# Kernel tuning notes

Hardware: AMD Instinct MI355X
Metric: run time of the kernel (lower is better)

The kernel has to match this reference:

```python
import jax, jax.numpy as jnp
import numpy as np

# Static config (must match init_kwargs)
IMG_H, IMG_W = 48, 160
BEV_H, BEV_W = 128, 128
X_MIN, X_MAX, Y_MIN, Y_MAX = -51.2, 51.2, -51.2, 51.2
RES_X = (X_MAX - X_MIN) / BEV_W
RES_Y = (Y_MAX - Y_MIN) / BEV_H
C, D, B = 128, 64, 2


def setup_inputs() -> dict:
    key = jax.random.key(0)
    k1, k2, k3, k4 = jax.random.split(key, 4)
    img_features = jax.random.normal(k1, (B, C, IMG_H, IMG_W), dtype=jnp.float32)
    # depth distribution per pixel (softmax over D, as a depth net would emit)
    depth_probs = jax.nn.softmax(jax.random.normal(k2, (B, D, IMG_H, IMG_W), dtype=jnp.float32), axis=1)
    # depth bin centers: 1m .. 60m
    depth_values = jnp.linspace(1.0, 60.0, D, dtype=jnp.float32)
    # realistic pinhole intrinsics (feature-map scale) with tiny per-cam jitter
    fx, fy, cx, cy = 120.0, 120.0, IMG_W / 2.0, IMG_H / 2.0
    K0 = jnp.array([[fx, 0.0, cx], [0.0, fy, cy], [0.0, 0.0, 1.0]], dtype=jnp.float32)
    K = K0[None] + 0.01 * jax.random.normal(k3, (B, 3, 3), dtype=jnp.float32) * jnp.array(
        [[1.0, 0.0, 1.0], [0.0, 1.0, 1.0], [0.0, 0.0, 0.0]], dtype=jnp.float32)
    # cam->lidar extrinsic: cam z (forward) -> lidar x, cam x -> -lidar y, cam y -> -lidar z
    R0 = jnp.array([[0.0, 0.0, 1.0], [-1.0, 0.0, 0.0], [0.0, -1.0, 0.0]], dtype=jnp.float32)
    t0 = jnp.array([1.5, 0.0, 1.8], dtype=jnp.float32)
    T0 = jnp.eye(4, dtype=jnp.float32).at[:3, :3].set(R0).at[:3, 3].set(t0)
    T = T0[None] + jnp.zeros((B, 4, 4), dtype=jnp.float32)
    T = T.at[:, :3, 3].add(0.05 * jax.random.normal(k4, (B, 3), dtype=jnp.float32))
    return {"img_features": img_features, "depth_probs": depth_probs,
            "depth_values": depth_values, "K": K, "T": T}


def _lss_forward(img_features, depth_probs, depth_values, K, T):
    Bn, Cn, H, W = img_features.shape
    Dn = depth_values.shape[0]
    # homogeneous pixel grid [H, W, 3]
    gx, gy = jnp.meshgrid(jnp.arange(W, dtype=jnp.float32),
                          jnp.arange(H, dtype=jnp.float32), indexing="xy")
    grid = jnp.stack([gx, gy, jnp.ones_like(gx)], axis=-1)
    # unproject: rays [B, H, W, 3]
    K_inv = jnp.linalg.inv(K)
    rays = jnp.einsum("bij,hwj->bhwi", K_inv, grid)
    # points in camera frame [B, D, H, W, 3]
    pts_cam = depth_values[None, :, None, None, None] * rays[:, None]
    # camera -> lidar
    pts = jnp.einsum("bij,bdhwj->bdhwi", T[:, :3, :3], pts_cam) + T[:, None, None, None, :3, 3]
    x, y, z = pts[..., 0], pts[..., 1], pts[..., 2]
    # torch .long() truncates toward zero -> astype int32 matches
    bx = ((x - X_MIN) / RES_X).astype(jnp.int32)
    by = ((y - Y_MIN) / RES_Y).astype(jnp.int32)
    valid = (bx >= 0) & (bx < BEV_W) & (by >= 0) & (by < BEV_H) & (z > 0)
    # depth-weighted features [B, D, H, W, C], masked instead of gathered
    weighted = jnp.einsum("bchw,bdhw->bdhwc", img_features, depth_probs)
    weighted = weighted * valid[..., None]
    idx = jnp.where(valid, by * BEV_W + bx, 0).reshape(Bn, -1)
    feats = weighted.reshape(Bn, -1, Cn)
    bev_flat = jax.vmap(lambda f, i: jax.ops.segment_sum(f, i, num_segments=BEV_H * BEV_W))(feats, idx)
    return bev_flat.reshape(Bn, BEV_H, BEV_W, Cn).transpose(0, 3, 1, 2)


def reference(img_features, depth_probs, depth_values, K, T):
    return _lss_forward(img_features, depth_probs, depth_values, K, T)
```

## Files before the change

kernel.cpp:

```cpp
#include <hip/hip_runtime.h>

constexpr int IMG_H = 48, IMG_W = 160;
constexpr int HW    = IMG_H * IMG_W;
constexpr int BEV_H = 128, BEV_W = 128;
constexpr int NCELL = BEV_H * BEV_W;
constexpr int C_DIM = 128, D_DIM = 64, B_DIM = 2;
constexpr int NCELL_TOT = B_DIM * NCELL;
constexpr int NPIX_TOT  = B_DIM * HW;
constexpr int NPTS      = NPIX_TOT * D_DIM;
constexpr int MAX_ENTRIES = NPTS;
constexpr int CHUNK = 64;
constexpr int NSHARD = 16;
constexpr float X_MIN = -51.2f, Y_MIN = -51.2f;
constexpr float RES_X = 102.4f / 128.0f;
constexpr float RES_Y = 102.4f / 128.0f;

constexpr size_t WS_IMG_T = 0;
constexpr size_t WS_HIST2 = WS_IMG_T + (size_t)B_DIM * HW * C_DIM;
constexpr size_t WS_OUT_T = WS_HIST2 + (size_t)NSHARD * NCELL_TOT;
constexpr size_t WS_HIST  = WS_OUT_T + (size_t)NCELL_TOT * C_DIM;
constexpr size_t WS_OFFS  = WS_HIST + NCELL_TOT;
constexpr size_t WS_EKEY  = WS_OFFS + NCELL_TOT + 4;
constexpr size_t WS_EW16  = WS_EKEY + MAX_ENTRIES;
constexpr size_t WS_NEED_CM = (WS_EW16 + MAX_ENTRIES / 2) * 4;

__device__ inline int point_shard(int tid) {
    return ((tid >> 2) + (tid >> 8)) & (NSHARD - 1);
}

__device__ inline void make_ray(const float* __restrict__ K, int b, float gx, float gy,
                                float& rx, float& ry, float& rz) {
    const float* Kb = K + b * 9;
    const float a00 = Kb[0], a01 = Kb[1], a02 = Kb[2];
    const float a10 = Kb[3], a11 = Kb[4], a12 = Kb[5];
    const float a20 = Kb[6], a21 = Kb[7], a22 = Kb[8];
    const float det = a00 * (a11 * a22 - a12 * a21)
                    - a01 * (a10 * a22 - a12 * a20)
                    + a02 * (a10 * a21 - a11 * a20);
    const float inv = 1.0f / det;
    const float i00 =  (a11 * a22 - a12 * a21) * inv;
    const float i01 = -(a01 * a22 - a02 * a21) * inv;
    const float i02 =  (a01 * a12 - a02 * a11) * inv;
    const float i10 = -(a10 * a22 - a12 * a20) * inv;
    const float i11 =  (a00 * a22 - a02 * a20) * inv;
    const float i12 = -(a00 * a12 - a02 * a10) * inv;
    const float i20 =  (a10 * a21 - a11 * a20) * inv;
    const float i21 = -(a00 * a21 - a01 * a20) * inv;
    const float i22 =  (a00 * a11 - a01 * a10) * inv;
    rx = i00 * gx + i01 * gy + i02;
    ry = i10 * gx + i11 * gy + i12;
    rz = i20 * gx + i21 * gy + i22;
}

__device__ inline int point_gcell(int tid, const float* __restrict__ dv,
                                  const float* __restrict__ K,
                                  const float* __restrict__ T) {
    const int pix = tid % HW;
    const int bd  = tid / HW;
    const int d   = bd % D_DIM;
    const int b   = bd / D_DIM;
    const int h = pix / IMG_W, w = pix % IMG_W;
    float rx, ry, rz;
    make_ray(K, b, (float)w, (float)h, rx, ry, rz);
    const float* Tb = T + b * 16;
    const float dep = dv[d];
    const float px = dep * rx, py = dep * ry, pz = dep * rz;
    const float x = Tb[0] * px + Tb[1] * py + Tb[2]  * pz + Tb[3];
    const float y = Tb[4] * px + Tb[5] * py + Tb[6]  * pz + Tb[7];
    const float z = Tb[8] * px + Tb[9] * py + Tb[10] * pz + Tb[11];
    const int bx = (int)((x - X_MIN) / RES_X);
    const int by = (int)((y - Y_MIN) / RES_Y);
    const bool valid = (bx >= 0) && (bx < BEV_W) && (by >= 0) && (by < BEV_H) && (z > 0.0f);
    return valid ? (b * NCELL + by * BEV_W + bx) : -1;
}

__device__ inline bool wave_runs(int gcell, int lane, int& run_len, int& leader_idx) {
    const int left = __shfl_up(gcell, 1);
    const bool is_leader = (lane == 0) || (left != gcell);
    const unsigned long long lmask = __ballot(is_leader);
    const unsigned long long rest = (lane == 63) ? 0ULL : (lmask >> (lane + 1));
    const int f = __ffsll((unsigned long long)rest);
    run_len = f ? f : (64 - lane);
    const unsigned long long below =
        lmask & ((lane == 63) ? ~0ULL : ((1ULL << (lane + 1)) - 1ULL));
    leader_idx = 63 - __clzll((long long)below);
    return is_leader;
}

__global__ __launch_bounds__(256) void k_transpose(const float* __restrict__ img,
                                                   float* __restrict__ img_t) {
    __shared__ float tile[32][33];
    const int b = blockIdx.z;
    const int tx = threadIdx.x, ty = threadIdx.y;
    const int pix0 = blockIdx.x * 32, c0 = blockIdx.y * 32;
    #pragma unroll
    for (int j = 0; j < 32; j += 8)
        tile[ty + j][tx] = img[((size_t)(b * C_DIM + c0 + ty + j)) * HW + pix0 + tx];
    __syncthreads();
    #pragma unroll
    for (int j = 0; j < 32; j += 8)
        img_t[((size_t)(b * HW + pix0 + ty + j)) * C_DIM + c0 + tx] = tile[tx][ty + j];
}

__global__ __launch_bounds__(256) void k_count(const float* __restrict__ dv,
                                               const float* __restrict__ K,
                                               const float* __restrict__ T,
                                               int* __restrict__ hist2) {
    const int tid = blockIdx.x * 256 + threadIdx.x;
    const int gcell = point_gcell(tid, dv, K, T);
    const int lane = threadIdx.x & 63;
    int run_len, leader_idx;
    const bool lead = wave_runs(gcell, lane, run_len, leader_idx);
    if (lead && gcell >= 0)
        atomicAdd(&hist2[(size_t)point_shard(tid) * NCELL_TOT + gcell], run_len);
}

__global__ __launch_bounds__(256) void k_reduce(const int* __restrict__ hist2,
                                                int* __restrict__ hist) {
    const int cell = blockIdx.x * 256 + threadIdx.x;
    int s = 0;
    #pragma unroll
    for (int sh = 0; sh < NSHARD; ++sh)
        s += hist2[(size_t)sh * NCELL_TOT + cell];
    hist[cell] = s;
}

__global__ __launch_bounds__(1024) void k_scan(const int* __restrict__ hist,
                                               int* __restrict__ offs) {
    __shared__ int lds[1024];
    const int t = threadIdx.x;
    int h[32];
    int s = 0;
    const int base = t * 32;
    #pragma unroll
    for (int k = 0; k < 32; ++k) { h[k] = hist[base + k]; s += h[k]; }
    lds[t] = s;
    __syncthreads();
    for (int off = 1; off < 1024; off <<= 1) {
        int v = (t >= off) ? lds[t - off] : 0;
        __syncthreads();
        lds[t] += v;
        __syncthreads();
    }
    int run = lds[t] - s;
    #pragma unroll
    for (int k = 0; k < 32; ++k) {
        offs[base + k] = run;
        run += h[k];
    }
    if (t == 1023) offs[NCELL_TOT] = lds[1023];
}

__global__ __launch_bounds__(256) void k_shardbase(int* __restrict__ hist2,
                                                   const int* __restrict__ offs) {
    const int cell = blockIdx.x * 256 + threadIdx.x;
    int run = offs[cell];
    #pragma unroll
    for (int sh = 0; sh < NSHARD; ++sh) {
        const size_t idx = (size_t)sh * NCELL_TOT + cell;
        const int cnt = hist2[idx];
        hist2[idx] = run;
        run += cnt;
    }
}

__global__ __launch_bounds__(256) void k_fill(const float* __restrict__ dp,
                                              const float* __restrict__ dv,
                                              const float* __restrict__ K,
                                              const float* __restrict__ T,
                                              int* __restrict__ cursor2,
                                              int* __restrict__ ekey,
                                              unsigned short* __restrict__ ew16) {
    const int tid = blockIdx.x * 256 + threadIdx.x;
    const int gcell = point_gcell(tid, dv, K, T);
    const int lane = threadIdx.x & 63;
    int run_len, leader_idx;
    const bool lead = wave_runs(gcell, lane, run_len, leader_idx);
    int base = 0;
    if (lead && gcell >= 0)
        base = atomicAdd(&cursor2[(size_t)point_shard(tid) * NCELL_TOT + gcell], run_len);
    base = __shfl(base, leader_idx);
    if (gcell < 0) return;
    const int slot = base + (lane - leader_idx);
    const float p = dp[tid];
    ekey[slot] = (gcell << 13) | (tid % HW);
    ew16[slot] = (unsigned short)__float2uint_rn(p * 65535.0f);
}

template <bool CELL_MAJOR>
__global__ __launch_bounds__(64) void k_chunk_gather(
    const float* __restrict__ img_t,
    const int* __restrict__ offs,
    const int* __restrict__ ekey,
    const unsigned short* __restrict__ ew16,
    float* __restrict__ acc_out)
{
    const int total = offs[NCELL_TOT];
    const int base = blockIdx.x * CHUNK;
    if (base >= total) return;

    __shared__ int   s_key[CHUNK];
    __shared__ float s_w[CHUNK];
    {
        const int i = threadIdx.x;
        const int idx = min(base + i, total - 1);
        s_key[i] = ekey[idx];
        s_w[i]   = (base + i < total) ? (float)ew16[base + i] * (1.0f / 65535.0f)
                                      : 0.0f;
    }
    __syncthreads();

    const int c2 = threadIdx.x * 2;
    int prev = s_key[0] >> 13;
    float2 acc = make_float2(0.0f, 0.0f);
    #pragma unroll 8
    for (int k = 0; k < CHUNK; ++k) {
        const int key = s_key[k];
        const float wgt = s_w[k];
        const int gcell = key >> 13;
        const int pix = key & 8191;
        const int b = gcell >> 14;
        const float2 v = *reinterpret_cast<const float2*>(
            &img_t[((size_t)(b * HW + pix)) * C_DIM + c2]);
        if (gcell != prev) {
            if (CELL_MAJOR) {
                float* o = &acc_out[(size_t)prev * C_DIM + c2];
                atomicAdd(o, acc.x);
                atomicAdd(o + 1, acc.y);
            } else {
                const int pb = prev >> 14, pc = prev & (NCELL - 1);
                float* o = &acc_out[((size_t)(pb * C_DIM + c2)) * NCELL + pc];
                atomicAdd(o, acc.x);
                atomicAdd(o + NCELL, acc.y);
            }
            acc = make_float2(0.0f, 0.0f);
            prev = gcell;
        }
        acc.x = fmaf(v.x, wgt, acc.x);
        acc.y = fmaf(v.y, wgt, acc.y);
    }
    if (CELL_MAJOR) {
        float* o = &acc_out[(size_t)prev * C_DIM + c2];
        atomicAdd(o, acc.x);
        atomicAdd(o + 1, acc.y);
    } else {
        const int pb = prev >> 14, pc = prev & (NCELL - 1);
        float* o = &acc_out[((size_t)(pb * C_DIM + c2)) * NCELL + pc];
        atomicAdd(o, acc.x);
        atomicAdd(o + NCELL, acc.y);
    }
}

__global__ __launch_bounds__(256) void k_untranspose(const float* __restrict__ out_t,
                                                     float* __restrict__ out) {
    __shared__ float tile[32][33];
    const int b = blockIdx.z;
    const int tx = threadIdx.x, ty = threadIdx.y;
    const int cell0 = blockIdx.x * 32, c0 = blockIdx.y * 32;
    const float* src = out_t + (size_t)b * NCELL * C_DIM;
    #pragma unroll
    for (int j = 0; j < 32; j += 8)
        tile[ty + j][tx] = src[((size_t)(cell0 + ty + j)) * C_DIM + c0 + tx];
    __syncthreads();
    #pragma unroll
    for (int j = 0; j < 32; j += 8)
        out[((size_t)(b * C_DIM + c0 + ty + j)) * NCELL + cell0 + tx] = tile[tx][ty + j];
}

extern "C" void kernel_launch(void* const* d_in, const int* in_sizes, int n_in,
                              void* d_out, int out_size, void* d_ws, size_t ws_size,
                              hipStream_t stream) {
    const float* img = (const float*)d_in[0];
    const float* dp  = (const float*)d_in[1];
    const float* dv  = (const float*)d_in[2];
    const float* K   = (const float*)d_in[3];
    const float* T   = (const float*)d_in[4];
    float* out = (float*)d_out;

    float* ws_f   = (float*)d_ws;
    float* img_t  = ws_f + WS_IMG_T;
    int*   hist2  = (int*)d_ws + WS_HIST2;
    float* out_t  = ws_f + WS_OUT_T;
    int*   hist   = (int*)d_ws + WS_HIST;
    int*   offs   = (int*)d_ws + WS_OFFS;
    int*   ekey   = (int*)d_ws + WS_EKEY;
    unsigned short* ew16 = (unsigned short*)((int*)d_ws + WS_EW16);

    const bool cell_major = (ws_size >= WS_NEED_CM);

    if (cell_major) {
        hipMemsetAsync(hist2, 0,
                       ((size_t)NSHARD * NCELL_TOT + (size_t)NCELL_TOT * C_DIM) * sizeof(int),
                       stream);
    } else {
        hipMemsetAsync(hist2, 0, (size_t)NSHARD * NCELL_TOT * sizeof(int), stream);
        hipMemsetAsync(out, 0, (size_t)out_size * sizeof(float), stream);
    }

    k_transpose<<<dim3(HW / 32, C_DIM / 32, B_DIM), dim3(32, 8), 0, stream>>>(img, img_t);
    k_count<<<NPTS / 256, 256, 0, stream>>>(dv, K, T, hist2);
    k_reduce<<<NCELL_TOT / 256, 256, 0, stream>>>(hist2, hist);
    k_scan<<<1, 1024, 0, stream>>>(hist, offs);
    k_shardbase<<<NCELL_TOT / 256, 256, 0, stream>>>(hist2, offs);
    k_fill<<<NPTS / 256, 256, 0, stream>>>(dp, dv, K, T, hist2, ekey, ew16);
    if (cell_major) {
        k_chunk_gather<true><<<MAX_ENTRIES / CHUNK, 64, 0, stream>>>(
            img_t, offs, ekey, ew16, out_t);
        k_untranspose<<<dim3(NCELL / 32, C_DIM / 32, B_DIM), dim3(32, 8), 0, stream>>>(
            out_t, out);
    } else {
        k_chunk_gather<false><<<MAX_ENTRIES / CHUNK, 64, 0, stream>>>(
            img_t, offs, ekey, ew16, out);
    }
}
```

Measured before the change: 164.7 us.

## Pre-merge depth bins per pixel ray and fuse transposes with counting

```diff
diff --git a/kernel.cpp b/kernel.cpp
--- a/kernel.cpp
+++ b/kernel.cpp
@@ -8,25 +8,22 @@
 constexpr int NCELL_TOT = B_DIM * NCELL;
 constexpr int NPIX_TOT  = B_DIM * HW;
 constexpr int NPTS      = NPIX_TOT * D_DIM;
-constexpr int MAX_ENTRIES = NPTS;
 constexpr int CHUNK = 64;
-constexpr int NSHARD = 16;
+constexpr int NSHARD = 64;
+constexpr int GATHER_BLOCKS = 3840;
+constexpr int CHUNKS_PER_BLOCK = NPTS / CHUNK / GATHER_BLOCKS;
 constexpr float X_MIN = -51.2f, Y_MIN = -51.2f;
 constexpr float RES_X = 102.4f / 128.0f;
 constexpr float RES_Y = 102.4f / 128.0f;
 
 constexpr size_t WS_IMG_T = 0;
-constexpr size_t WS_HIST2 = WS_IMG_T + (size_t)B_DIM * HW * C_DIM;
+constexpr size_t WS_DP_T  = WS_IMG_T + (size_t)B_DIM * HW * C_DIM;
+constexpr size_t WS_HIST2 = WS_DP_T + (size_t)B_DIM * HW * D_DIM;
 constexpr size_t WS_OUT_T = WS_HIST2 + (size_t)NSHARD * NCELL_TOT;
 constexpr size_t WS_HIST  = WS_OUT_T + (size_t)NCELL_TOT * C_DIM;
 constexpr size_t WS_OFFS  = WS_HIST + NCELL_TOT;
 constexpr size_t WS_EKEY  = WS_OFFS + NCELL_TOT + 4;
-constexpr size_t WS_EW16  = WS_EKEY + MAX_ENTRIES;
-constexpr size_t WS_NEED_CM = (WS_EW16 + MAX_ENTRIES / 2) * 4;
-
-__device__ inline int point_shard(int tid) {
-    return ((tid >> 2) + (tid >> 8)) & (NSHARD - 1);
-}
+constexpr size_t WS_EW16  = WS_EKEY + NPTS;
 
 __device__ inline void make_ray(const float* __restrict__ K, int b, float gx, float gy,
                                 float& rx, float& ry, float& rz) {
@@ -52,13 +49,10 @@
     rz = i20 * gx + i21 * gy + i22;
 }
 
-__device__ inline int point_gcell(int tid, const float* __restrict__ dv,
-                                  const float* __restrict__ K,
-                                  const float* __restrict__ T) {
-    const int pix = tid % HW;
-    const int bd  = tid / HW;
-    const int d   = bd % D_DIM;
-    const int b   = bd / D_DIM;
+__device__ inline int gcell_ray(int b, int pix, int d,
+                                const float* __restrict__ dv,
+                                const float* __restrict__ K,
+                                const float* __restrict__ T) {
     const int h = pix / IMG_W, w = pix % IMG_W;
     float rx, ry, rz;
     make_ray(K, b, (float)w, (float)h, rx, ry, rz);
@@ -74,45 +68,61 @@
     return valid ? (b * NCELL + by * BEV_W + bx) : -1;
 }
 
-__device__ inline bool wave_runs(int gcell, int lane, int& run_len, int& leader_idx) {
+struct RunInfo { int leader_idx; bool is_tail; };
+__device__ inline RunInfo wave_runs_d(int gcell, int lane) {
     const int left = __shfl_up(gcell, 1);
     const bool is_leader = (lane == 0) || (left != gcell);
     const unsigned long long lmask = __ballot(is_leader);
-    const unsigned long long rest = (lane == 63) ? 0ULL : (lmask >> (lane + 1));
-    const int f = __ffsll((unsigned long long)rest);
-    run_len = f ? f : (64 - lane);
     const unsigned long long below =
         lmask & ((lane == 63) ? ~0ULL : ((1ULL << (lane + 1)) - 1ULL));
-    leader_idx = 63 - __clzll((long long)below);
-    return is_leader;
-}
-
-__global__ __launch_bounds__(256) void k_transpose(const float* __restrict__ img,
-                                                   float* __restrict__ img_t) {
-    __shared__ float tile[32][33];
-    const int b = blockIdx.z;
-    const int tx = threadIdx.x, ty = threadIdx.y;
-    const int pix0 = blockIdx.x * 32, c0 = blockIdx.y * 32;
-    #pragma unroll
-    for (int j = 0; j < 32; j += 8)
-        tile[ty + j][tx] = img[((size_t)(b * C_DIM + c0 + ty + j)) * HW + pix0 + tx];
-    __syncthreads();
-    #pragma unroll
-    for (int j = 0; j < 32; j += 8)
-        img_t[((size_t)(b * HW + pix0 + ty + j)) * C_DIM + c0 + tx] = tile[tx][ty + j];
-}
-
-__global__ __launch_bounds__(256) void k_count(const float* __restrict__ dv,
-                                               const float* __restrict__ K,
-                                               const float* __restrict__ T,
-                                               int* __restrict__ hist2) {
-    const int tid = blockIdx.x * 256 + threadIdx.x;
-    const int gcell = point_gcell(tid, dv, K, T);
-    const int lane = threadIdx.x & 63;
-    int run_len, leader_idx;
-    const bool lead = wave_runs(gcell, lane, run_len, leader_idx);
-    if (lead && gcell >= 0)
-        atomicAdd(&hist2[(size_t)point_shard(tid) * NCELL_TOT + gcell], run_len);
+    RunInfo r;
+    r.leader_idx = 63 - __clzll((long long)below);
+    r.is_tail = (lane == 63) || ((lmask >> (lane + 1)) & 1ULL);
+    return r;
+}
+
+__device__ inline int shard_of(int pix) { return (pix ^ (pix >> 6)) & (NSHARD - 1); }
+
+constexpr int NB_IMG = (HW / 32) * (C_DIM / 32) * B_DIM;
+constexpr int NB_DP  = (HW / 32) * (D_DIM / 32) * B_DIM;
+constexpr int NB_CNT = NPTS / 256;
+__global__ __launch_bounds__(256) void k_prep(const float* __restrict__ img,
+                                              const float* __restrict__ dp,
+                                              const float* __restrict__ dv,
+                                              const float* __restrict__ K,
+                                              const float* __restrict__ T,
+                                              float* __restrict__ img_t,
+                                              float* __restrict__ dp_t,
+                                              int* __restrict__ hist2) {
+    int bid = blockIdx.x;
+    if (bid < NB_IMG + NB_DP) {
+        const float* src; float* dst; int rows;
+        if (bid < NB_IMG) { src = img; dst = img_t; rows = C_DIM; }
+        else              { bid -= NB_IMG; src = dp; dst = dp_t; rows = D_DIM; }
+        const int tiles_c = rows / 32;
+        const int b = bid / ((HW / 32) * tiles_c);
+        const int r = bid % ((HW / 32) * tiles_c);
+        const int ctile = r / (HW / 32), ptile = r % (HW / 32);
+        __shared__ float tile[32][33];
+        const int tx = threadIdx.x & 31, ty = threadIdx.x >> 5;
+        const int pix0 = ptile * 32, c0 = ctile * 32;
+        #pragma unroll
+        for (int j = 0; j < 32; j += 8)
+            tile[ty + j][tx] = src[((size_t)(b * rows + c0 + ty + j)) * HW + pix0 + tx];
+        __syncthreads();
+        #pragma unroll
+        for (int j = 0; j < 32; j += 8)
+            dst[((size_t)(b * HW + pix0 + ty + j)) * rows + c0 + tx] = tile[tx][ty + j];
+    } else {
+        const int tid = (bid - NB_IMG - NB_DP) * 256 + threadIdx.x;
+        const int lane = threadIdx.x & 63;
+        const int wid = tid >> 6;
+        const int b = wid / HW, pix = wid % HW;
+        const int gcell = gcell_ray(b, pix, lane, dv, K, T);
+        const RunInfo ri = wave_runs_d(gcell, lane);
+        if (ri.is_tail && gcell >= 0)
+            atomicAdd(&hist2[(size_t)shard_of(pix) * NCELL_TOT + gcell], 1);
+    }
 }
 
 __global__ __launch_bounds__(256) void k_reduce(const int* __restrict__ hist2,
@@ -164,7 +174,7 @@
     }
 }
 
-__global__ __launch_bounds__(256) void k_fill(const float* __restrict__ dp,
+__global__ __launch_bounds__(256) void k_fill(const float* __restrict__ dp_t,
                                               const float* __restrict__ dv,
                                               const float* __restrict__ K,
                                               const float* __restrict__ T,
@@ -172,82 +182,77 @@
                                               int* __restrict__ ekey,
                                               unsigned short* __restrict__ ew16) {
     const int tid = blockIdx.x * 256 + threadIdx.x;
-    const int gcell = point_gcell(tid, dv, K, T);
     const int lane = threadIdx.x & 63;
-    int run_len, leader_idx;
-    const bool lead = wave_runs(gcell, lane, run_len, leader_idx);
-    int base = 0;
-    if (lead && gcell >= 0)
-        base = atomicAdd(&cursor2[(size_t)point_shard(tid) * NCELL_TOT + gcell], run_len);
-    base = __shfl(base, leader_idx);
-    if (gcell < 0) return;
-    const int slot = base + (lane - leader_idx);
-    const float p = dp[tid];
-    ekey[slot] = (gcell << 13) | (tid % HW);
-    ew16[slot] = (unsigned short)__float2uint_rn(p * 65535.0f);
-}
-
-template <bool CELL_MAJOR>
-__global__ __launch_bounds__(64) void k_chunk_gather(
+    const int wid = tid >> 6;
+    const int b = wid / HW, pix = wid % HW;
+    const int gcell = gcell_ray(b, pix, lane, dv, K, T);
+    const RunInfo ri = wave_runs_d(gcell, lane);
+    const float p = dp_t[((size_t)(b * HW + pix)) * D_DIM + lane];
+    float val = p;
+    #pragma unroll
+    for (int dlt = 1; dlt < 64; dlt <<= 1) {
+        const float up = __shfl_up(val, dlt);
+        val = (lane - dlt >= ri.leader_idx) ? val + up : val;
+    }
+    if (ri.is_tail && gcell >= 0) {
+        const int slot = atomicAdd(&cursor2[(size_t)shard_of(pix) * NCELL_TOT + gcell], 1);
+        ekey[slot] = (gcell << 13) | pix;
+        ew16[slot] = (unsigned short)__float2uint_rn(fminf(val * 65535.0f, 65535.0f));
+    }
+}
+
+__global__ __launch_bounds__(64) void k_gather(
     const float* __restrict__ img_t,
     const int* __restrict__ offs,
     const int* __restrict__ ekey,
     const unsigned short* __restrict__ ew16,
-    float* __restrict__ acc_out)
+    float* __restrict__ out_t)
 {
     const int total = offs[NCELL_TOT];
-    const int base = blockIdx.x * CHUNK;
-    if (base >= total) return;
-
     __shared__ int   s_key[CHUNK];
     __shared__ float s_w[CHUNK];
-    {
-        const int i = threadIdx.x;
-        const int idx = min(base + i, total - 1);
-        s_key[i] = ekey[idx];
-        s_w[i]   = (base + i < total) ? (float)ew16[base + i] * (1.0f / 65535.0f)
-                                      : 0.0f;
-    }
-    __syncthreads();
 
     const int c2 = threadIdx.x * 2;
-    int prev = s_key[0] >> 13;
+    int prev = -1;
     float2 acc = make_float2(0.0f, 0.0f);
-    #pragma unroll 8
-    for (int k = 0; k < CHUNK; ++k) {
-        const int key = s_key[k];
-        const float wgt = s_w[k];
-        const int gcell = key >> 13;
-        const int pix = key & 8191;
-        const int b = gcell >> 14;
-        const float2 v = *reinterpret_cast<const float2*>(
-            &img_t[((size_t)(b * HW + pix)) * C_DIM + c2]);
-        if (gcell != prev) {
-            if (CELL_MAJOR) {
-                float* o = &acc_out[(size_t)prev * C_DIM + c2];
+
+    for (int cc = 0; cc < CHUNKS_PER_BLOCK; ++cc) {
+        const int base = (blockIdx.x * CHUNKS_PER_BLOCK + cc) * CHUNK;
+        if (base >= total) break;
+        __syncthreads();
+        {
+            const int i = threadIdx.x;
+            const int idx = min(base + i, total - 1);
+            s_key[i] = ekey[idx];
+            s_w[i]   = (base + i < total) ? (float)ew16[base + i] * (1.0f / 65535.0f)
+                                          : 0.0f;
+        }
+        __syncthreads();
+        if (prev < 0) prev = s_key[0] >> 13;
+        #pragma unroll 8
+        for (int k = 0; k < CHUNK; ++k) {
+            const int key = s_key[k];
+            const float wgt = s_w[k];
+            const int gcell = key >> 13;
+            const int pix = key & 8191;
+            const int b = gcell >> 14;
+            const float2 v = *reinterpret_cast<const float2*>(
+                &img_t[((size_t)(b * HW + pix)) * C_DIM + c2]);
+            if (gcell != prev) {
+                float* o = &out_t[(size_t)prev * C_DIM + c2];
                 atomicAdd(o, acc.x);
                 atomicAdd(o + 1, acc.y);
-            } else {
-                const int pb = prev >> 14, pc = prev & (NCELL - 1);
-                float* o = &acc_out[((size_t)(pb * C_DIM + c2)) * NCELL + pc];
-                atomicAdd(o, acc.x);
-                atomicAdd(o + NCELL, acc.y);
+                acc = make_float2(0.0f, 0.0f);
+                prev = gcell;
             }
-            acc = make_float2(0.0f, 0.0f);
-            prev = gcell;
+            acc.x = fmaf(v.x, wgt, acc.x);
+            acc.y = fmaf(v.y, wgt, acc.y);
         }
-        acc.x = fmaf(v.x, wgt, acc.x);
-        acc.y = fmaf(v.y, wgt, acc.y);
-    }
-    if (CELL_MAJOR) {
-        float* o = &acc_out[(size_t)prev * C_DIM + c2];
+    }
+    if (prev >= 0) {
+        float* o = &out_t[(size_t)prev * C_DIM + c2];
         atomicAdd(o, acc.x);
         atomicAdd(o + 1, acc.y);
-    } else {
-        const int pb = prev >> 14, pc = prev & (NCELL - 1);
-        float* o = &acc_out[((size_t)(pb * C_DIM + c2)) * NCELL + pc];
-        atomicAdd(o, acc.x);
-        atomicAdd(o + NCELL, acc.y);
     }
 }
 
@@ -279,6 +284,7 @@
 
     float* ws_f   = (float*)d_ws;
     float* img_t  = ws_f + WS_IMG_T;
+    float* dp_t   = ws_f + WS_DP_T;
     int*   hist2  = (int*)d_ws + WS_HIST2;
     float* out_t  = ws_f + WS_OUT_T;
     int*   hist   = (int*)d_ws + WS_HIST;
@@ -286,30 +292,17 @@
     int*   ekey   = (int*)d_ws + WS_EKEY;
     unsigned short* ew16 = (unsigned short*)((int*)d_ws + WS_EW16);
 
-    const bool cell_major = (ws_size >= WS_NEED_CM);
-
-    if (cell_major) {
-        hipMemsetAsync(hist2, 0,
-                       ((size_t)NSHARD * NCELL_TOT + (size_t)NCELL_TOT * C_DIM) * sizeof(int),
-                       stream);
-    } else {
-        hipMemsetAsync(hist2, 0, (size_t)NSHARD * NCELL_TOT * sizeof(int), stream);
-        hipMemsetAsync(out, 0, (size_t)out_size * sizeof(float), stream);
-    }
-
-    k_transpose<<<dim3(HW / 32, C_DIM / 32, B_DIM), dim3(32, 8), 0, stream>>>(img, img_t);
-    k_count<<<NPTS / 256, 256, 0, stream>>>(dv, K, T, hist2);
+    hipMemsetAsync(hist2, 0,
+                   ((size_t)NSHARD * NCELL_TOT + (size_t)NCELL_TOT * C_DIM) * sizeof(int),
+                   stream);
+
+    k_prep<<<NB_IMG + NB_DP + NB_CNT, 256, 0, stream>>>(img, dp, dv, K, T,
+                                                        img_t, dp_t, hist2);
     k_reduce<<<NCELL_TOT / 256, 256, 0, stream>>>(hist2, hist);
     k_scan<<<1, 1024, 0, stream>>>(hist, offs);
     k_shardbase<<<NCELL_TOT / 256, 256, 0, stream>>>(hist2, offs);
-    k_fill<<<NPTS / 256, 256, 0, stream>>>(dp, dv, K, T, hist2, ekey, ew16);
-    if (cell_major) {
-        k_chunk_gather<true><<<MAX_ENTRIES / CHUNK, 64, 0, stream>>>(
-            img_t, offs, ekey, ew16, out_t);
-        k_untranspose<<<dim3(NCELL / 32, C_DIM / 32, B_DIM), dim3(32, 8), 0, stream>>>(
-            out_t, out);
-    } else {
-        k_chunk_gather<false><<<MAX_ENTRIES / CHUNK, 64, 0, stream>>>(
-            img_t, offs, ekey, ew16, out);
-    }
-}
+    k_fill<<<NPTS / 256, 256, 0, stream>>>(dp_t, dv, K, T, hist2, ekey, ew16);
+    k_gather<<<GATHER_BLOCKS, 64, 0, stream>>>(img_t, offs, ekey, ew16, out_t);
+    k_untranspose<<<dim3(NCELL / 32, C_DIM / 32, B_DIM), dim3(32, 8), 0, stream>>>(
+        out_t, out);
+}
```

After: 190.8 us. 1.16x slower.
